# Kernel optimization log

Hardware: AMD Instinct MI355X
Metric: run time of the kernel (lower is better)

## Reference

```python
import jax, jax.numpy as jnp
import numpy as np

E = 768      # embed_dim (hidden_size)
H = 12       # num_attention_heads
DH = E // H  # head_dim = 64
B, S = 8, 1024


def setup_inputs() -> dict:
    key = jax.random.key(0)
    ks = jax.random.split(key, 10)
    sc = 1.0 / np.sqrt(E)
    inp = {
        "hidden_state": jax.random.normal(ks[0], (B, S, E), dtype=jnp.float32),
        # per-head Q/K/V projections, stacked over heads: [H, E, DH]
        "Wq": jax.random.normal(ks[1], (H, E, DH), dtype=jnp.float32) * sc,
        "bq": jax.random.normal(ks[2], (H, DH), dtype=jnp.float32) * 0.02,
        "Wk": jax.random.normal(ks[3], (H, E, DH), dtype=jnp.float32) * sc,
        "bk": jax.random.normal(ks[4], (H, DH), dtype=jnp.float32) * 0.02,
        "Wv": jax.random.normal(ks[5], (H, E, DH), dtype=jnp.float32) * sc,
        "bv": jax.random.normal(ks[6], (H, DH), dtype=jnp.float32) * 0.02,
        # output projection: [E, E]
        "Wo": jax.random.normal(ks[7], (E, E), dtype=jnp.float32) * sc,
        "bo": jax.random.normal(ks[8], (E,), dtype=jnp.float32) * 0.02,
    }
    return inp


def reference(hidden_state, Wq, bq, Wk, bk, Wv, bv, Wo, bo):
    # Q/K/V per head: [B,S,E] x [H,E,D] -> [B,H,S,D]
    q = jnp.einsum("bse,hed->bhsd", hidden_state, Wq) + bq[None, :, None, :]
    k = jnp.einsum("bse,hed->bhsd", hidden_state, Wk) + bk[None, :, None, :]
    v = jnp.einsum("bse,hed->bhsd", hidden_state, Wv) + bv[None, :, None, :]
    scale = 1.0 / jnp.sqrt(jnp.asarray(DH, dtype=q.dtype))
    scores = jnp.einsum("bhsd,bhtd->bhst", q, k) * scale   # [B,H,S,S]
    weights = jax.nn.softmax(scores, axis=-1)
    attn = jnp.einsum("bhst,bhtd->bhsd", weights, v)        # [B,H,S,D]
    # concat heads (head order matches ModuleList concat): [B,S,H*D]=[B,S,E]
    x = attn.transpose(0, 2, 1, 3).reshape(hidden_state.shape[0], hidden_state.shape[1], E)
    return x @ Wo + bo
```

## Files before the change

kernel.cpp:

```cpp
#include <hip/hip_runtime.h>

typedef unsigned short u16;
typedef __bf16 bf16;
typedef bf16 bf16x8 __attribute__((ext_vector_type(8)));
typedef float f32x4 __attribute__((ext_vector_type(4)));
typedef u16 u16x4 __attribute__((ext_vector_type(4)));
typedef u16 u16x8 __attribute__((ext_vector_type(8)));

#define MROWS 8192
#define EDIM 768
#define NQKV 2304
#define NHEAD 12
#define DH 64
#define SEQ 1024
#define BATCH 8
#define BH 96
#define BHSD (BH * SEQ * DH)

__device__ __forceinline__ u16 f2bf(float f) {
  union { float f; unsigned u; } v; v.f = f;
  unsigned r = v.u + 0x7fffu + ((v.u >> 16) & 1u);
  return (u16)(r >> 16);
}

#define GLDS16(g, l)                                                          \
  __builtin_amdgcn_global_load_lds(                                           \
      (const __attribute__((address_space(1))) void*)(g),                     \
      (__attribute__((address_space(3))) void*)(l), 16, 0, 0)


__global__ void cvt_x(const float* __restrict__ x, u16* __restrict__ xb, int n) {
  int i = (blockIdx.x * blockDim.x + threadIdx.x) * 4;
  if (i >= n) return;
  float4 v = *(const float4*)(x + i);
  u16x4 o;
  o[0] = f2bf(v.x); o[1] = f2bf(v.y); o[2] = f2bf(v.z); o[3] = f2bf(v.w);
  *(u16x4*)(xb + i) = o;
}

__global__ void pack_w(const float* __restrict__ Wq, const float* __restrict__ Wk,
                       const float* __restrict__ Wv, const float* __restrict__ Wo,
                       u16* __restrict__ Wt, u16* __restrict__ Wot) {
  int idx = blockIdx.x * blockDim.x + threadIdx.x;
  if (idx < NQKV * EDIM) {
    int n = idx / EDIM, e = idx - n * EDIM;
    int region = n / EDIM;
    int hd = n - region * EDIM;
    int h = hd >> 6, d = hd & 63;
    const float* W = region == 0 ? Wq : (region == 1 ? Wk : Wv);
    Wt[idx] = f2bf(W[(h * EDIM + e) * DH + d]);
  }
  if (idx < EDIM * EDIM) {
    int n = idx / EDIM, e = idx - n * EDIM;
    Wot[idx] = f2bf(Wo[e * EDIM + n]);
  }
}

__device__ __forceinline__ void gemm_core(
    const u16* __restrict__ A, const u16* __restrict__ Bt,
    u16* As, u16* Bs, int m0, int n0, int tid, f32x4 acc[4][4]) {
  int wv = __builtin_amdgcn_readfirstlane(tid >> 6);
  int lane = tid & 63, quad = lane >> 4, l16 = lane & 15;
  int wm = (wv & 1) * 64, wn = (wv >> 1) * 64;
  int srow = wv * 32 + (lane >> 2);
  int schunk = (lane & 3) ^ ((lane >> 3) & 3);
  const u16* Ag = A + (size_t)(m0 + srow) * EDIM + schunk * 8;
  const u16* Bg = Bt + (size_t)(n0 + srow) * EDIM + schunk * 8;
  u16* Asb = As + wv * 32 * 32;
  u16* Bsb = Bs + wv * 32 * 32;
  int fragoff = (quad ^ ((l16 >> 1) & 3)) * 8;

  for (int k0 = 0; k0 < EDIM; k0 += 32) {
    __syncthreads();
    GLDS16(Ag + k0, Asb);
    GLDS16(Ag + k0 + 16 * EDIM, Asb + 16 * 32);
    GLDS16(Bg + k0, Bsb);
    GLDS16(Bg + k0 + 16 * EDIM, Bsb + 16 * 32);
    __syncthreads();
    bf16x8 af[4], bfr[4];
    for (int i = 0; i < 4; i++)
      af[i] = *(const bf16x8*)(As + (wm + i * 16 + l16) * 32 + fragoff);
    for (int j = 0; j < 4; j++)
      bfr[j] = *(const bf16x8*)(Bs + (wn + j * 16 + l16) * 32 + fragoff);
    for (int i = 0; i < 4; i++)
      for (int j = 0; j < 4; j++)
        acc[i][j] = __builtin_amdgcn_mfma_f32_16x16x32_bf16(af[i], bfr[j], acc[i][j], 0, 0, 0);
  }
}

__global__ __launch_bounds__(256, 4) void gemm_qkv(
    const u16* __restrict__ A, const u16* __restrict__ Bt,
    const float* __restrict__ bq, const float* __restrict__ bk, const float* __restrict__ bv,
    u16* __restrict__ qkv) {
  __shared__ u16 As[128 * 32];
  __shared__ u16 Bs[128 * 32];
  int tid = threadIdx.x;
  int wv = tid >> 6, lane = tid & 63, quad = lane >> 4, l16 = lane & 15;
  int wm = (wv & 1) * 64, wn = (wv >> 1) * 64;
  int m0 = blockIdx.x * 128, n0 = blockIdx.y * 128;
  f32x4 acc[4][4] = {};
  gemm_core(A, Bt, As, Bs, m0, n0, tid, acc);

  const float kQscale = 0.18033688011112042f;
  for (int i = 0; i < 4; i++) {
    int row0 = m0 + wm + i * 16 + quad * 4;
    for (int j = 0; j < 4; j++) {
      int n = n0 + wn + j * 16 + l16;
      int region = n / EDIM;
      int hd = n - region * EDIM;
      int h = hd >> 6, d = hd & 63;
      const float* bp = region == 0 ? bq : (region == 1 ? bk : bv);
      float bias = bp[hd];
      float scale = region == 0 ? kQscale : 1.0f;
      for (int r = 0; r < 4; r++) {
        int rr = row0 + r;
        int bb = rr >> 10, s = rr & 1023;
        float val = (acc[i][j][r] + bias) * scale;
        u16 bv16 = f2bf(val);
        int bhh = bb * NHEAD + h;
        if (region < 2) {
          qkv[(size_t)region * BHSD + ((size_t)bhh * SEQ + s) * DH + d] = bv16;
        } else {
          qkv[(size_t)2 * BHSD + ((size_t)bhh * DH + d) * SEQ + s] = bv16;
        }
      }
    }
  }
}

__global__ __launch_bounds__(256) void attn_kernel(const u16* __restrict__ qkv, u16* __restrict__ attn) {
  int bh = blockIdx.y;
  int b = bh / NHEAD, h = bh - b * NHEAD;
  const u16* Q  = qkv + (size_t)bh * SEQ * DH;
  const u16* K  = qkv + (size_t)(BH + bh) * SEQ * DH;
  const u16* VT = qkv + (size_t)(2 * BH + bh) * SEQ * DH;
  int tid = threadIdx.x, wave = tid >> 6, lane = tid & 63, quad = lane >> 4, l16 = lane & 15;
  int q_base = blockIdx.x * 128 + wave * 32;

  __shared__ u16 Ks[32 * 72];
  __shared__ u16 Vts[64 * 40];
  __shared__ u16 Ps[4][32 * 40];

  bf16x8 qf[2][2];
  for (int qi = 0; qi < 2; qi++)
    for (int c = 0; c < 2; c++)
      qf[qi][c] = *(const bf16x8*)(Q + (size_t)(q_base + qi * 16 + l16) * DH + c * 32 + quad * 8);

  f32x4 o[2][4] = {};
  float l_i[2][4] = {};

  int tr = tid >> 3, tc8 = (tid & 7) * 8;
  int vr = tid >> 2, vc8 = (tid & 3) * 8;

  for (int t0 = 0; t0 < SEQ; t0 += 32) {
    u16x8 kv = *(const u16x8*)(K + (size_t)(t0 + tr) * DH + tc8);
    u16x8 vv = *(const u16x8*)(VT + (size_t)vr * SEQ + t0 + vc8);
    __syncthreads();
    *(u16x8*)(Ks + tr * 72 + tc8) = kv;
    *(u16x8*)(Vts + vr * 40 + vc8) = vv;
    __syncthreads();

    bf16x8 kf[2][2];
    for (int tc = 0; tc < 2; tc++)
      for (int c = 0; c < 2; c++)
        kf[tc][c] = *(const bf16x8*)(Ks + (tc * 16 + l16) * 72 + c * 32 + quad * 8);

    float p[2][2][4];
    for (int qi = 0; qi < 2; qi++)
      for (int tc = 0; tc < 2; tc++) {
        f32x4 z = {};
        z = __builtin_amdgcn_mfma_f32_16x16x32_bf16(qf[qi][0], kf[tc][0], z, 0, 0, 0);
        z = __builtin_amdgcn_mfma_f32_16x16x32_bf16(qf[qi][1], kf[tc][1], z, 0, 0, 0);
        for (int r = 0; r < 4; r++) {
          float e = exp2f(z[r]);
          p[qi][tc][r] = e;
          l_i[qi][r] += e;
        }
      }

    u16* P = Ps[wave];
    for (int qi = 0; qi < 2; qi++)
      for (int tc = 0; tc < 2; tc++)
        for (int r = 0; r < 4; r++)
          P[(qi * 16 + quad * 4 + r) * 40 + tc * 16 + l16] = f2bf(p[qi][tc][r]);
    bf16x8 pf[2];
    for (int qi = 0; qi < 2; qi++)
      pf[qi] = *(const bf16x8*)(P + (qi * 16 + l16) * 40 + quad * 8);

    bf16x8 vf[4];
    for (int n = 0; n < 4; n++)
      vf[n] = *(const bf16x8*)(Vts + (n * 16 + l16) * 40 + quad * 8);

    for (int qi = 0; qi < 2; qi++)
      for (int n = 0; n < 4; n++)
        o[qi][n] = __builtin_amdgcn_mfma_f32_16x16x32_bf16(pf[qi], vf[n], o[qi][n], 0, 0, 0);
  }

  for (int qi = 0; qi < 2; qi++)
    for (int r = 0; r < 4; r++) {
      float s = l_i[qi][r];
      for (int mask = 1; mask <= 8; mask <<= 1)
        s += __shfl_xor(s, mask);
      l_i[qi][r] = s;
    }

  for (int qi = 0; qi < 2; qi++)
    for (int r = 0; r < 4; r++) {
      float inv = 1.0f / l_i[qi][r];
      int qrow = q_base + qi * 16 + quad * 4 + r;
      size_t rowoff = (size_t)(b * SEQ + qrow) * EDIM + h * DH;
      for (int n = 0; n < 4; n++)
        attn[rowoff + n * 16 + l16] = f2bf(o[qi][n][r] * inv);
    }
}

__global__ __launch_bounds__(256, 4) void gemm_out(
    const u16* __restrict__ A, const u16* __restrict__ Bt,
    const float* __restrict__ bo, float* __restrict__ out) {
  __shared__ u16 As[128 * 32];
  __shared__ u16 Bs[128 * 32];
  int tid = threadIdx.x;
  int wv = tid >> 6, lane = tid & 63, quad = lane >> 4, l16 = lane & 15;
  int wm = (wv & 1) * 64, wn = (wv >> 1) * 64;
  int m0 = blockIdx.x * 128, n0 = blockIdx.y * 128;
  f32x4 acc[4][4] = {};
  gemm_core(A, Bt, As, Bs, m0, n0, tid, acc);

  for (int i = 0; i < 4; i++) {
    int row0 = m0 + wm + i * 16 + quad * 4;
    for (int j = 0; j < 4; j++) {
      int n = n0 + wn + j * 16 + l16;
      float bias = bo[n];
      for (int r = 0; r < 4; r++)
        out[(size_t)(row0 + r) * EDIM + n] = acc[i][j][r] + bias;
    }
  }
}

extern "C" void kernel_launch(void* const* d_in, const int* in_sizes, int n_in,
                              void* d_out, int out_size, void* d_ws, size_t ws_size,
                              hipStream_t stream) {
  const float* x  = (const float*)d_in[0];
  const float* Wq = (const float*)d_in[1];
  const float* bq = (const float*)d_in[2];
  const float* Wk = (const float*)d_in[3];
  const float* bk = (const float*)d_in[4];
  const float* Wv = (const float*)d_in[5];
  const float* bv = (const float*)d_in[6];
  const float* Wo = (const float*)d_in[7];
  const float* bo = (const float*)d_in[8];
  float* out = (float*)d_out;
  char* ws = (char*)d_ws;

  u16* Xb   = (u16*)(ws);
  u16* Wt   = (u16*)(ws + 12582912);
  u16* Wot  = (u16*)(ws + 16121856);
  u16* qkv  = (u16*)(ws + 17301504);
  u16* attn = (u16*)(ws + 55050240);

  cvt_x<<<6144, 256, 0, stream>>>(x, Xb, MROWS * EDIM);
  pack_w<<<6912, 256, 0, stream>>>(Wq, Wk, Wv, Wo, Wt, Wot);
  gemm_qkv<<<dim3(64, 18), 256, 0, stream>>>(Xb, Wt, bq, bk, bv, qkv);
  attn_kernel<<<dim3(8, 96), 256, 0, stream>>>(qkv, attn);
  gemm_out<<<dim3(64, 6), 256, 0, stream>>>(attn, Wot, bo, out);
}
```

Baseline: 237.6 us.

## Double-buffer GEMM LDS tiles and transpose weights through shared-memory tiles

The shared GEMM core now keeps two LDS buffers and issues global-to-LDS loads for the next K slice before running MFMAs on the current one. This removes the second barrier per iteration and overlaps memory latency with compute. The weight-packing kernel becomes a 64x64 tiled transpose through padded shared memory, so both its global reads and writes are coalesced instead of strided. In exchange, each GEMM block uses twice as much LDS, which could lower occupancy.

Result: faster. 228.7 us (-3.7%).

```diff
diff --git a/kernel.cpp b/kernel.cpp
--- a/kernel.cpp
+++ b/kernel.cpp
@@ -16,6 +16,8 @@
 #define BATCH 8
 #define BH 96
 #define BHSD (BH * SEQ * DH)
+#define KITERS (EDIM / 32)
+#define TBUF (128 * 32)
 
 __device__ __forceinline__ u16 f2bf(float f) {
   union { float f; unsigned u; } v; v.f = f;
@@ -38,27 +40,47 @@
   *(u16x4*)(xb + i) = o;
 }
 
-__global__ void pack_w(const float* __restrict__ Wq, const float* __restrict__ Wk,
-                       const float* __restrict__ Wv, const float* __restrict__ Wo,
-                       u16* __restrict__ Wt, u16* __restrict__ Wot) {
-  int idx = blockIdx.x * blockDim.x + threadIdx.x;
-  if (idx < NQKV * EDIM) {
-    int n = idx / EDIM, e = idx - n * EDIM;
-    int region = n / EDIM;
-    int hd = n - region * EDIM;
-    int h = hd >> 6, d = hd & 63;
+__global__ __launch_bounds__(256) void pack_w(
+    const float* __restrict__ Wq, const float* __restrict__ Wk,
+    const float* __restrict__ Wv, const float* __restrict__ Wo,
+    u16* __restrict__ Wt, u16* __restrict__ Wot) {
+  __shared__ float T[64][65];
+  int bid = blockIdx.x;
+  int tid = threadIdx.x;
+  int c = tid & 63, r4 = tid >> 6;
+  if (bid < 432) {
+    int region = bid / 144, rem = bid - region * 144;
+    int h = rem / 12, e0 = (rem - h * 12) * 64;
     const float* W = region == 0 ? Wq : (region == 1 ? Wk : Wv);
-    Wt[idx] = f2bf(W[(h * EDIM + e) * DH + d]);
-  }
-  if (idx < EDIM * EDIM) {
-    int n = idx / EDIM, e = idx - n * EDIM;
-    Wot[idx] = f2bf(Wo[e * EDIM + n]);
+    for (int p = 0; p < 16; p++) {
+      int er = r4 + p * 4;
+      T[er][c] = W[(size_t)(h * EDIM + e0 + er) * DH + c];
+    }
+    __syncthreads();
+    int nbase = region * EDIM + h * 64;
+    for (int p = 0; p < 16; p++) {
+      int dr = r4 + p * 4;
+      Wt[(size_t)(nbase + dr) * EDIM + e0 + c] = f2bf(T[c][dr]);
+    }
+  } else {
+    bid -= 432;
+    int n0 = (bid / 12) * 64, e0 = (bid - (bid / 12) * 12) * 64;
+    for (int p = 0; p < 16; p++) {
+      int er = r4 + p * 4;
+      T[er][c] = Wo[(size_t)(e0 + er) * EDIM + n0 + c];
+    }
+    __syncthreads();
+    for (int p = 0; p < 16; p++) {
+      int dr = r4 + p * 4;
+      Wot[(size_t)(n0 + dr) * EDIM + e0 + c] = f2bf(T[c][dr]);
+    }
   }
 }
 
 __device__ __forceinline__ void gemm_core(
     const u16* __restrict__ A, const u16* __restrict__ Bt,
-    u16* As, u16* Bs, int m0, int n0, int tid, f32x4 acc[4][4]) {
+    u16* As, u16* Bs,
+    int m0, int n0, int tid, f32x4 acc[4][4]) {
   int wv = __builtin_amdgcn_readfirstlane(tid >> 6);
   int lane = tid & 63, quad = lane >> 4, l16 = lane & 15;
   int wm = (wv & 1) * 64, wn = (wv >> 1) * 64;
@@ -66,22 +88,29 @@
   int schunk = (lane & 3) ^ ((lane >> 3) & 3);
   const u16* Ag = A + (size_t)(m0 + srow) * EDIM + schunk * 8;
   const u16* Bg = Bt + (size_t)(n0 + srow) * EDIM + schunk * 8;
-  u16* Asb = As + wv * 32 * 32;
-  u16* Bsb = Bs + wv * 32 * 32;
+  int sboff = wv * 32 * 32;
   int fragoff = (quad ^ ((l16 >> 1) & 3)) * 8;
 
-  for (int k0 = 0; k0 < EDIM; k0 += 32) {
-    __syncthreads();
-    GLDS16(Ag + k0, Asb);
-    GLDS16(Ag + k0 + 16 * EDIM, Asb + 16 * 32);
-    GLDS16(Bg + k0, Bsb);
-    GLDS16(Bg + k0 + 16 * EDIM, Bsb + 16 * 32);
-    __syncthreads();
+  GLDS16(Ag, As + sboff);
+  GLDS16(Ag + 16 * EDIM, As + sboff + 16 * 32);
+  GLDS16(Bg, Bs + sboff);
+  GLDS16(Bg + 16 * EDIM, Bs + sboff + 16 * 32);
+
+  for (int k = 0; k < KITERS; k++) {
+    int cur = (k & 1) * TBUF, nxt = ((k + 1) & 1) * TBUF;
+    __syncthreads();
+    if (k + 1 < KITERS) {
+      int ko = (k + 1) * 32;
+      GLDS16(Ag + ko, As + nxt + sboff);
+      GLDS16(Ag + ko + 16 * EDIM, As + nxt + sboff + 16 * 32);
+      GLDS16(Bg + ko, Bs + nxt + sboff);
+      GLDS16(Bg + ko + 16 * EDIM, Bs + nxt + sboff + 16 * 32);
+    }
     bf16x8 af[4], bfr[4];
     for (int i = 0; i < 4; i++)
-      af[i] = *(const bf16x8*)(As + (wm + i * 16 + l16) * 32 + fragoff);
+      af[i] = *(const bf16x8*)(As + cur + (wm + i * 16 + l16) * 32 + fragoff);
     for (int j = 0; j < 4; j++)
-      bfr[j] = *(const bf16x8*)(Bs + (wn + j * 16 + l16) * 32 + fragoff);
+      bfr[j] = *(const bf16x8*)(Bs + cur + (wn + j * 16 + l16) * 32 + fragoff);
     for (int i = 0; i < 4; i++)
       for (int j = 0; j < 4; j++)
         acc[i][j] = __builtin_amdgcn_mfma_f32_16x16x32_bf16(af[i], bfr[j], acc[i][j], 0, 0, 0);
@@ -92,8 +121,8 @@
     const u16* __restrict__ A, const u16* __restrict__ Bt,
     const float* __restrict__ bq, const float* __restrict__ bk, const float* __restrict__ bv,
     u16* __restrict__ qkv) {
-  __shared__ u16 As[128 * 32];
-  __shared__ u16 Bs[128 * 32];
+  __shared__ u16 As[2 * TBUF];
+  __shared__ u16 Bs[2 * TBUF];
   int tid = threadIdx.x;
   int wv = tid >> 6, lane = tid & 63, quad = lane >> 4, l16 = lane & 15;
   int wm = (wv & 1) * 64, wn = (wv >> 1) * 64;
@@ -217,8 +246,8 @@
 __global__ __launch_bounds__(256, 4) void gemm_out(
     const u16* __restrict__ A, const u16* __restrict__ Bt,
     const float* __restrict__ bo, float* __restrict__ out) {
-  __shared__ u16 As[128 * 32];
-  __shared__ u16 Bs[128 * 32];
+  __shared__ u16 As[2 * TBUF];
+  __shared__ u16 Bs[2 * TBUF];
   int tid = threadIdx.x;
   int wv = tid >> 6, lane = tid & 63, quad = lane >> 4, l16 = lane & 15;
   int wm = (wv & 1) * 64, wn = (wv >> 1) * 64;
@@ -259,7 +288,7 @@
   u16* attn = (u16*)(ws + 55050240);
 
   cvt_x<<<6144, 256, 0, stream>>>(x, Xb, MROWS * EDIM);
-  pack_w<<<6912, 256, 0, stream>>>(Wq, Wk, Wv, Wo, Wt, Wot);
+  pack_w<<<576, 256, 0, stream>>>(Wq, Wk, Wv, Wo, Wt, Wot);
   gemm_qkv<<<dim3(64, 18), 256, 0, stream>>>(Xb, Wt, bq, bk, bv, qkv);
   attn_kernel<<<dim3(8, 96), 256, 0, stream>>>(qkv, attn);
   gemm_out<<<dim3(64, 6), 256, 0, stream>>>(attn, Wot, bo, out);
```
